# Kernel optimization log

Hardware: AMD Instinct MI355X
Metric: run time of the kernel (lower is better)

The kernel has to match this reference:

```python
import jax, jax.numpy as jnp
import numpy as np

B, L, D = 4, 8192, 512


def _normalize(v):
    # F.normalize: v / max(||v||, 1e-12)
    n = jnp.linalg.norm(v, axis=-1, keepdims=True)
    return v / jnp.maximum(n, 1e-12)


def setup_inputs() -> dict:
    key = jax.random.key(0)
    k1, k2, k3, k4 = jax.random.split(key, 4)
    return {
        "hidden_states": jax.random.normal(k1, (B, L, D), jnp.float32),
        "residual": jax.random.normal(k2, (B, L, D), jnp.float32),
        "q_weight": jax.random.normal(k3, (D, D), jnp.float32) * 0.02,
        "k_weight": jax.random.normal(k4, (D, D), jnp.float32) * 0.02,
        "det_state": jnp.zeros((B, D), jnp.float32),
    }


def reference(hidden_states, residual, q_weight, k_weight, det_state):
    Bs, Ls, Ds = hidden_states.shape
    # ---- CosineSimRouter.prob_boundary ----
    q = _normalize(hidden_states[:, :-1] @ q_weight.T)   # (B, L-1, D)
    k = _normalize(hidden_states[:, 1:] @ k_weight.T)    # (B, L-1, D)
    cos_sim = jnp.einsum('bld,bld->bl', q, k)            # (B, L-1)
    prob = jnp.concatenate(
        [jnp.ones((Bs, 1), jnp.float32), jnp.clip((1.0 - cos_sim) / 2.0, 0.0, 1.0)],
        axis=1)                                           # (B, L); prob[:,0]=1 (state=None path)
    token_mask = prob > 0.5                               # (B, L)

    # ---- Tokenizer: compact boundary positions (pad M -> L, static shape) ----
    counts = token_mask.sum(axis=1)                       # (B,)
    order = jnp.argsort(~token_mask, axis=1)              # stable: True-mask indices first, in order
    valid = jnp.arange(Ls)[None, :] < counts[:, None]     # (B, L)
    chunked = jnp.take_along_axis(hidden_states, order[..., None], axis=1)
    chunked = chunked * valid[..., None]                  # (B, L, D)
    chunk_probs = jnp.take_along_axis(prob, order, axis=1) * valid  # (B, L)

    # ---- DeTokenizer: EMA associative scan over compacted chunks ----
    decay = jnp.clip(1.0 - chunk_probs, 0.0, 1.0)
    # pad positions have chunk_probs=0 -> decay=1 -> state carried unchanged
    a = jnp.broadcast_to(decay[..., None], (Bs, Ls, Ds))
    b = (1.0 - decay)[..., None] * chunked
    b = b.at[:, 0].add(a[:, 0] * det_state)

    def comb(x, y):  # x earlier, y later: (a2*a1, a2*b1 + b2)
        ax, bx = x
        ay, by = y
        return ax * ay, ay * bx + by

    _, ema_out = jax.lax.associative_scan(comb, (a, b), axis=1)
    ema_out = ema_out * valid[..., None]                  # zero padded chunk slots

    # broadcast back to full sequence via cumulative chunk indexing
    chunk_idx = jnp.cumsum(token_mask.astype(jnp.int32), axis=1) - 1  # (B, L)
    ci = jnp.clip(chunk_idx, 0, Ls - 1)
    long_states = jnp.take_along_axis(ema_out, ci[..., None], axis=1)
    long_states = long_states * (chunk_idx >= 0)[..., None]

    # STE coefficient: forward == 1 (grad flows through max(1-p, p) in bwd)
    coef_raw = jnp.maximum(1.0 - prob, prob)
    coef = coef_raw + jax.lax.stop_gradient(1.0 - coef_raw)
    long_states = long_states * coef[..., None]

    output = residual + long_states                       # (B, L, D)
    return output
```

## Files before the change

### kernel.cpp

```cpp
#include <hip/hip_runtime.h>
#include <hip/hip_bf16.h>
#include <math.h>

#define B_  4
#define L_  8192
#define D_  512

#define BM   128
#define NCT  4
#define NRT  (L_ / BM)
#define KW   64
#define NSTAGE (D_ / KW)

#define CHUNK 64
#define NCHUNK (L_ / CHUNK)

#define MAXFIX 16380
#define FIX_TAU 1.0e-3f
#define FTILE 4

typedef short bf16x8 __attribute__((ext_vector_type(8)));
typedef float f32x4 __attribute__((ext_vector_type(4)));
typedef unsigned short u16;
typedef unsigned int u32;

__device__ __forceinline__ u32 pk2(float lo, float hi) {
    __hip_bfloat162 v = __float22bfloat162_rn(float2{lo, hi});
    union { __hip_bfloat162 b; u32 u; } cv; cv.b = v;
    return cv.u;
}

__global__ __launch_bounds__(256) void prep_w(
    const float* __restrict__ wq, const float* __restrict__ wk,
    u16* __restrict__ qh, u16* __restrict__ kh,
    float* __restrict__ wqt, float* __restrict__ wkt,
    int* __restrict__ fix_cnt)
{
    __shared__ float tile[64][65];
    const int bi = blockIdx.x;
    const int bj = blockIdx.y;
    const int t = threadIdx.x;
    if (bi == 0 && bj == 0 && t == 0) *fix_cnt = 0;
    const int c0 = bi * 64, k0 = bj * 64;
    const float* src = wq; float* dst = wqt; u16* dsth = qh;
#pragma unroll
    for (int m = 0; m < 2; ++m) {
        __syncthreads();
#pragma unroll
        for (int it = 0; it < 4; ++it) {
            int r = it * 16 + (t >> 4);
            int cc = (t & 15) * 4;
            float4 v = *(const float4*)(src + (size_t)(c0 + r) * D_ + k0 + cc);
            tile[r][cc] = v.x; tile[r][cc + 1] = v.y;
            tile[r][cc + 2] = v.z; tile[r][cc + 3] = v.w;
            uint2 hv; hv.x = pk2(v.x, v.y); hv.y = pk2(v.z, v.w);
            *(uint2*)(dsth + (size_t)(c0 + r) * D_ + k0 + cc) = hv;
        }
        __syncthreads();
#pragma unroll
        for (int it = 0; it < 4; ++it) {
            int cl = t & 63;
            int kq = it * 4 + (t >> 6);
            float4 v;
            v.x = tile[cl][kq * 4 + 0]; v.y = tile[cl][kq * 4 + 1];
            v.z = tile[cl][kq * 4 + 2]; v.w = tile[cl][kq * 4 + 3];
            size_t o = ((size_t)((k0 >> 2) + kq) * 512 + (c0 + cl)) * 4;
            *(float4*)(dst + o) = v;
        }
        src = wk; dst = wkt; dsth = kh;
    }
}

__global__ __launch_bounds__(256, 2) void qk_mfma(
    const float* __restrict__ h,
    const u16* __restrict__ wqh, const u16* __restrict__ wkh,
    float* __restrict__ part)
{
    const int bid = blockIdx.x;
    const int swz = (bid & 7) * 128 + (bid >> 3);
    const int ct = swz & 3, rt = (swz >> 2) & 63, b = swz >> 8;
    const int t = threadIdx.x, wid = t >> 6, lane = t & 63;
    const int l15 = lane & 15, l4 = lane >> 4;

    __shared__ __align__(16) u16 ah[129 * 64];
    __shared__ float red[4][BM][3];

    const int r0 = rt * BM;
    const float* hb = h + (size_t)b * L_ * D_;

    const int tr = t >> 4, q = t & 15;
    const float* gp = hb + (size_t)(r0 + tr) * D_ + q * 4;
    const int re = (r0 + BM > L_ - 1) ? (L_ - 1) : (r0 + BM);
    const float* gpe = hb + (size_t)re * D_ + q * 4;
    const int dbase = tr * 64 + (((q >> 1) ^ (tr & 7)) * 8) + ((q & 1) * 4);
    const int dE = 128 * 64 + ((t >> 1) * 8) + ((t & 1) * 4);

    const int colb = ct * 128 + wid * 32;
    const u16* bq0 = wqh + (size_t)(colb + l15) * D_ + l4 * 8;
    const u16* bq1 = bq0 + (size_t)16 * D_;
    const u16* bk0 = wkh + (size_t)(colb + l15) * D_ + l4 * 8;
    const u16* bk1 = bk0 + (size_t)16 * D_;

    int aoff[8];
#pragma unroll
    for (int rf = 0; rf < 8; ++rf) {
        int R = rf * 16 + l15;
        aoff[rf] = R * 64 + ((l4 ^ (R & 7)) * 8);
    }
    const int aoffE = 128 * 64 + l4 * 8;

    f32x4 accq[8][2], acck[8][2], ackl[2];
    const f32x4 zero = {0.f, 0.f, 0.f, 0.f};
#pragma unroll
    for (int rf = 0; rf < 8; ++rf) {
        accq[rf][0] = zero; accq[rf][1] = zero;
        acck[rf][0] = zero; acck[rf][1] = zero;
    }
    ackl[0] = zero; ackl[1] = zero;

    float4 A0, A1, A2, A3, A4, A5, A6, A7;
    float4 AE = {0.f, 0.f, 0.f, 0.f};

#define LOADA(S) do { const int _o = (S) * KW;                      \
    A0 = *(const float4*)(gp + _o);                                 \
    A1 = *(const float4*)(gp + _o + 8192);                          \
    A2 = *(const float4*)(gp + _o + 16384);                         \
    A3 = *(const float4*)(gp + _o + 24576);                         \
    A4 = *(const float4*)(gp + _o + 32768);                         \
    A5 = *(const float4*)(gp + _o + 40960);                         \
    A6 = *(const float4*)(gp + _o + 49152);                         \
    A7 = *(const float4*)(gp + _o + 57344);                         \
    if (t < 16) AE = *(const float4*)(gpe + _o); } while (0)

#define ST1(J, AV) { uint2 _h; _h.x = pk2(AV.x, AV.y); _h.y = pk2(AV.z, AV.w); \
    *(uint2*)(&ah[dbase + (J) * 1024]) = _h; }

    LOADA(0);
    for (int s = 0; s < NSTAGE; ++s) {
        __syncthreads();
        ST1(0, A0) ST1(1, A1) ST1(2, A2) ST1(3, A3)
        ST1(4, A4) ST1(5, A5) ST1(6, A6) ST1(7, A7)
        if (t < 16) { uint2 _h; _h.x = pk2(AE.x, AE.y); _h.y = pk2(AE.z, AE.w);
                      *(uint2*)(&ah[dE]) = _h; }

        const int so = s * KW;
        bf16x8 q00 = *(const bf16x8*)(bq0 + so);
        bf16x8 q01 = *(const bf16x8*)(bq0 + so + 32);
        bf16x8 q10 = *(const bf16x8*)(bq1 + so);
        bf16x8 q11 = *(const bf16x8*)(bq1 + so + 32);
        bf16x8 k00 = *(const bf16x8*)(bk0 + so);
        bf16x8 k01 = *(const bf16x8*)(bk0 + so + 32);
        bf16x8 k10 = *(const bf16x8*)(bk1 + so);
        bf16x8 k11 = *(const bf16x8*)(bk1 + so + 32);

        if (s + 1 < NSTAGE) LOADA(s + 1);
        __syncthreads();

#pragma unroll
        for (int kk = 0; kk < 2; ++kk) {
            bf16x8 fq0 = kk ? q01 : q00;
            bf16x8 fq1 = kk ? q11 : q10;
            bf16x8 fk0 = kk ? k01 : k00;
            bf16x8 fk1 = kk ? k11 : k10;
#pragma unroll
            for (int rf = 0; rf < 8; ++rf) {
                bf16x8 a = *(const bf16x8*)(&ah[aoff[rf] ^ (kk * 32)]);
                accq[rf][0] = __builtin_amdgcn_mfma_f32_16x16x32_bf16(a, fq0, accq[rf][0], 0, 0, 0);
                accq[rf][1] = __builtin_amdgcn_mfma_f32_16x16x32_bf16(a, fq1, accq[rf][1], 0, 0, 0);
                acck[rf][0] = __builtin_amdgcn_mfma_f32_16x16x32_bf16(a, fk0, acck[rf][0], 0, 0, 0);
                acck[rf][1] = __builtin_amdgcn_mfma_f32_16x16x32_bf16(a, fk1, acck[rf][1], 0, 0, 0);
            }
            bf16x8 al = *(const bf16x8*)(&ah[aoffE ^ (kk * 32)]);
            ackl[0] = __builtin_amdgcn_mfma_f32_16x16x32_bf16(al, fk0, ackl[0], 0, 0, 0);
            ackl[1] = __builtin_amdgcn_mfma_f32_16x16x32_bf16(al, fk1, ackl[1], 0, 0, 0);
        }
    }
#undef LOADA
#undef ST1

#pragma unroll
    for (int rf = 0; rf < 8; ++rf) {
#pragma unroll
        for (int reg = 0; reg < 4; ++reg) {
            float pq = 0.f, pk = 0.f, pd = 0.f;
#pragma unroll
            for (int cf = 0; cf < 2; ++cf) {
                float qv = accq[rf][cf][reg];
                float kv = acck[rf][cf][reg];
                pq += qv * qv;
                pk += kv * kv;
                float ksh;
                if (reg < 3) {
                    ksh = acck[rf][cf][reg + 1];
                } else {
                    float up = __shfl(acck[rf][cf][0], (lane + 16) & 63);
                    float nx0 = (rf < 7) ? acck[rf + 1][cf][0] : ackl[cf][0];
                    float nx = __shfl(nx0, l15);
                    ksh = (l4 == 3) ? nx : up;
                }
                pd += qv * ksh;
            }
#pragma unroll
            for (int off = 1; off < 16; off <<= 1) {
                pq += __shfl_xor(pq, off);
                pk += __shfl_xor(pk, off);
                pd += __shfl_xor(pd, off);
            }
            if (l15 == 0) {
                int row = rf * 16 + l4 * 4 + reg;
                red[wid][row][0] = pq;
                red[wid][row][1] = pk;
                red[wid][row][2] = pd;
            }
        }
    }
    __syncthreads();
    if (t < BM) {
        float pq = red[0][t][0] + red[1][t][0] + red[2][t][0] + red[3][t][0];
        float pk = red[0][t][1] + red[1][t][1] + red[2][t][1] + red[3][t][1];
        float pd = red[0][t][2] + red[1][t][2] + red[2][t][2] + red[3][t][2];
        size_t o = (((size_t)ct * B_ + b) * L_ + (r0 + t)) * 3;
        part[o + 0] = pq; part[o + 1] = pk; part[o + 2] = pd;
    }
}

__global__ __launch_bounds__(256) void cos_reduce(
    const float* __restrict__ part, float* __restrict__ p,
    int* __restrict__ fix_cnt, int* __restrict__ fix_list)
{
    int idx = blockIdx.x * 256 + threadIdx.x;
    if (idx >= B_ * L_) return;
    int b = idx / L_;
    int tp = idx % L_;
    if (tp == 0) { p[idx] = 1.0f; return; }
    int l = tp - 1;
    float nq = 0.f, nk = 0.f, dt = 0.f;
#pragma unroll
    for (int ct = 0; ct < NCT; ++ct) {
        size_t o = (((size_t)ct * B_ + b) * L_ + l) * 3;
        nq += part[o + 0];
        dt += part[o + 2];
        nk += part[o + 4];
    }
    float qn = sqrtf(nq); if (qn < 1e-12f) qn = 1e-12f;
    float kn = sqrtf(nk); if (kn < 1e-12f) kn = 1e-12f;
    float cs = dt / (qn * kn);
    float pr = 0.5f * (1.0f - cs);
    pr = fminf(fmaxf(pr, 0.0f), 1.0f);
    p[idx] = pr;
    if (fabsf(cs) < FIX_TAU) {
        int slot = atomicAdd(fix_cnt, 1);
        if (slot < MAXFIX) fix_list[slot] = idx;
    }
}

__global__ __launch_bounds__(256) void fixup_main(
    const float* __restrict__ h,
    const float* __restrict__ wqt, const float* __restrict__ wkt,
    const int* __restrict__ fix_cnt, const int* __restrict__ fix_list,
    float* __restrict__ p)
{
    __shared__ float hq[FTILE][D_];
    __shared__ float hk[FTILE][D_];
    __shared__ float red[FTILE][3][4];
    const int t = threadIdx.x, wid = t >> 6, lane = t & 63;
    int n = *fix_cnt; if (n > MAXFIX) n = MAXFIX;
    const int ntiles = (n + FTILE - 1) / FTILE;

    for (int tile = blockIdx.x; tile < ntiles; tile += gridDim.x) {
        __syncthreads();
#pragma unroll
        for (int r = 0; r < FTILE; ++r) {
            int s = tile * FTILE + r;
            int idx = fix_list[s < n ? s : 0];
            int bb = idx >> 13;
            int tp = idx & (L_ - 1);
            const float* hr = h + ((size_t)bb * L_ + (tp - 1)) * D_;
            ((float2*)hq[r])[t] = ((const float2*)hr)[t];
            ((float2*)hk[r])[t] = ((const float2*)(hr + D_))[t];
        }
        __syncthreads();

        float qa0[FTILE], qa1[FTILE], ka0[FTILE], ka1[FTILE];
#pragma unroll
        for (int r = 0; r < FTILE; ++r) { qa0[r] = qa1[r] = ka0[r] = ka1[r] = 0.f; }

        float4 wc0 = *(const float4*)(wqt + ((size_t)0 * 512 + t) * 4);
        float4 wc1 = *(const float4*)(wqt + ((size_t)0 * 512 + t + 256) * 4);
        float4 xc0 = *(const float4*)(wkt + ((size_t)0 * 512 + t) * 4);
        float4 xc1 = *(const float4*)(wkt + ((size_t)0 * 512 + t + 256) * 4);
#pragma unroll 4
        for (int kq = 0; kq < D_ / 4; ++kq) {
            const int kn = (kq + 1) & (D_ / 4 - 1);
            float4 wn0 = *(const float4*)(wqt + ((size_t)kn * 512 + t) * 4);
            float4 wn1 = *(const float4*)(wqt + ((size_t)kn * 512 + t + 256) * 4);
            float4 xn0 = *(const float4*)(wkt + ((size_t)kn * 512 + t) * 4);
            float4 xn1 = *(const float4*)(wkt + ((size_t)kn * 512 + t + 256) * 4);
#pragma unroll
            for (int r = 0; r < FTILE; ++r) {
                float4 hv = *(const float4*)(&hq[r][kq * 4]);
                float4 kv = *(const float4*)(&hk[r][kq * 4]);
                qa0[r] += hv.x * wc0.x + hv.y * wc0.y + hv.z * wc0.z + hv.w * wc0.w;
                qa1[r] += hv.x * wc1.x + hv.y * wc1.y + hv.z * wc1.z + hv.w * wc1.w;
                ka0[r] += kv.x * xc0.x + kv.y * xc0.y + kv.z * xc0.z + kv.w * xc0.w;
                ka1[r] += kv.x * xc1.x + kv.y * xc1.y + kv.z * xc1.z + kv.w * xc1.w;
            }
            wc0 = wn0; wc1 = wn1; xc0 = xn0; xc1 = xn1;
        }

#pragma unroll
        for (int r = 0; r < FTILE; ++r) {
            float pq = qa0[r] * qa0[r] + qa1[r] * qa1[r];
            float pk = ka0[r] * ka0[r] + ka1[r] * ka1[r];
            float pd = qa0[r] * ka0[r] + qa1[r] * ka1[r];
#pragma unroll
            for (int off = 1; off < 64; off <<= 1) {
                pq += __shfl_xor(pq, off);
                pk += __shfl_xor(pk, off);
                pd += __shfl_xor(pd, off);
            }
            if (lane == 0) { red[r][0][wid] = pq; red[r][1][wid] = pk; red[r][2][wid] = pd; }
        }
        __syncthreads();
        if (t < FTILE) {
            int s = tile * FTILE + t;
            if (s < n) {
                float nq = red[t][0][0] + red[t][0][1] + red[t][0][2] + red[t][0][3];
                float nk = red[t][1][0] + red[t][1][1] + red[t][1][2] + red[t][1][3];
                float dt = red[t][2][0] + red[t][2][1] + red[t][2][2] + red[t][2][3];
                float qn = sqrtf(nq); if (qn < 1e-12f) qn = 1e-12f;
                float kn = sqrtf(nk); if (kn < 1e-12f) kn = 1e-12f;
                float cs = dt / (qn * kn);
                float pr = 0.5f * (1.0f - cs);
                pr = fminf(fmaxf(pr, 0.0f), 1.0f);
                p[fix_list[s]] = pr;
            }
        }
    }
}

__global__ __launch_bounds__(256) void scan_a(
    const float* __restrict__ h, const float* __restrict__ p,
    float* __restrict__ Bc, float* __restrict__ Ac)
{
    const int t = threadIdx.x;
    const int c = blockIdx.x, b = blockIdx.y;
    const int l0 = c * CHUNK;
    const float* pb = p + (size_t)b * L_ + l0;
    const float2* hb = (const float2*)(h + ((size_t)b * L_ + l0) * D_) + t;

    float2 st = {0.f, 0.f};
    float ap = 1.f;
#pragma unroll 4
    for (int i = 0; i < CHUNK; ++i) {
        float pr = pb[i];
        float2 hv = hb[(size_t)i * 256];
        bool sel = pr > 0.5f;
        float a = sel ? 1.f - pr : 1.f;
        float g = sel ? pr : 0.f;
        st.x = a * st.x + g * hv.x;
        st.y = a * st.y + g * hv.y;
        ap *= a;
    }
    ((float2*)Bc)[((size_t)b * NCHUNK + c) * 256 + t] = st;
    if (t == 0) Ac[b * NCHUNK + c] = ap;
}

__global__ __launch_bounds__(256) void scan_b(
    const float* __restrict__ Ac, const float* __restrict__ Bc,
    const float* __restrict__ det, float* __restrict__ carry)
{
    const int t = threadIdx.x;
    const int b = blockIdx.x;
    const float* acb = Ac + b * NCHUNK;
    const float2* bcb = (const float2*)Bc + (size_t)b * NCHUNK * 256 + t;
    float2* cb = (float2*)carry + (size_t)b * NCHUNK * 256 + t;
    float2 st = ((const float2*)det)[(size_t)b * 256 + t];

    float a0 = acb[0], a1 = acb[1], a2 = acb[2], a3 = acb[3];
    float2 b0 = bcb[0], b1 = bcb[256], b2 = bcb[512], b3 = bcb[768];
    for (int g = 0; g < NCHUNK / 4; ++g) {
        const int nc = (g + 1 < NCHUNK / 4) ? (g + 1) * 4 : g * 4;
        float an0 = acb[nc], an1 = acb[nc + 1], an2 = acb[nc + 2], an3 = acb[nc + 3];
        float2 bn0 = bcb[(size_t)nc * 256],        bn1 = bcb[(size_t)(nc + 1) * 256];
        float2 bn2 = bcb[(size_t)(nc + 2) * 256],  bn3 = bcb[(size_t)(nc + 3) * 256];
        const size_t c0 = (size_t)g * 4 * 256;
        cb[c0]       = st; st.x = a0 * st.x + b0.x; st.y = a0 * st.y + b0.y;
        cb[c0 + 256] = st; st.x = a1 * st.x + b1.x; st.y = a1 * st.y + b1.y;
        cb[c0 + 512] = st; st.x = a2 * st.x + b2.x; st.y = a2 * st.y + b2.y;
        cb[c0 + 768] = st; st.x = a3 * st.x + b3.x; st.y = a3 * st.y + b3.y;
        a0 = an0; a1 = an1; a2 = an2; a3 = an3;
        b0 = bn0; b1 = bn1; b2 = bn2; b3 = bn3;
    }
}

__global__ __launch_bounds__(256) void scan_c(
    const float* __restrict__ h, const float* __restrict__ p,
    const float* __restrict__ res, const float* __restrict__ carry,
    float* __restrict__ out)
{
    const int t = threadIdx.x;
    const int c = blockIdx.x, b = blockIdx.y;
    const int l0 = c * CHUNK;
    const float* pb = p + (size_t)b * L_ + l0;
    const size_t base = ((size_t)b * L_ + l0) * 256 + t;
    const float2* hb = (const float2*)h + base;
    const float2* rb = (const float2*)res + base;
    float2* ob = (float2*)out + base;

    float2 st = ((const float2*)carry)[((size_t)b * NCHUNK + c) * 256 + t];
#pragma unroll 4
    for (int i = 0; i < CHUNK; ++i) {
        float pr = pb[i];
        float2 hv = hb[(size_t)i * 256];
        float2 rv = rb[(size_t)i * 256];
        bool sel = pr > 0.5f;
        float a = sel ? 1.f - pr : 1.f;
        float g = sel ? pr : 0.f;
        st.x = a * st.x + g * hv.x;
        st.y = a * st.y + g * hv.y;
        float2 ov; ov.x = rv.x + st.x; ov.y = rv.y + st.y;
        ob[(size_t)i * 256] = ov;
    }
}

extern "C" void kernel_launch(void* const* d_in, const int* in_sizes, int n_in,
                              void* d_out, int out_size, void* d_ws, size_t ws_size,
                              hipStream_t stream)
{
    const float* h   = (const float*)d_in[0];
    const float* res = (const float*)d_in[1];
    const float* wq  = (const float*)d_in[2];
    const float* wk  = (const float*)d_in[3];
    const float* det = (const float*)d_in[4];
    float* out = (float*)d_out;

    float* ws = (float*)d_ws;
    float* part  = ws;
    float* p     = part + (size_t)NCT * B_ * L_ * 3;
    float* Ac    = p + (size_t)B_ * L_;
    float* Bc    = Ac + (size_t)B_ * NCHUNK;
    float* carry = Bc + (size_t)B_ * NCHUNK * D_;
    int*  fix_cnt  = (int*)(carry + (size_t)B_ * NCHUNK * D_);
    int*  fix_list = fix_cnt + 4;
    u16* wqh = (u16*)(fix_list + MAXFIX);
    u16* wkh = wqh + (size_t)D_ * D_;
    float* wqt = (float*)(wkh + (size_t)D_ * D_);
    float* wkt = wqt + (size_t)D_ * D_;

    prep_w<<<dim3(8, 8), 256, 0, stream>>>(wq, wk, wqh, wkh, wqt, wkt, fix_cnt);
    qk_mfma<<<NCT * NRT * B_, 256, 0, stream>>>(h, wqh, wkh, part);
    cos_reduce<<<(B_ * L_ + 255) / 256, 256, 0, stream>>>(part, p, fix_cnt, fix_list);
    fixup_main<<<256, 256, 0, stream>>>(h, wqt, wkt, fix_cnt, fix_list, p);
    scan_a<<<dim3(NCHUNK, B_), 256, 0, stream>>>(h, p, Bc, Ac);
    scan_b<<<B_, 256, 0, stream>>>(Ac, Bc, det, carry);
    scan_c<<<dim3(NCHUNK, B_), 256, 0, stream>>>(h, p, res, carry, out);
}
```

Measured before the change: 201.7 us.

## Tune fixup tiling, software-pipeline weight loads, relax barriers, prefetch weights into cache

Several changes at once. The fixup kernel now processes 8 rows per tile on half as many blocks and uses a 4-deep rotating register pipeline for weight loads. The MFMA kernel swaps __syncthreads for raw s_barrier with an explicit lgkmcnt wait and sched barriers. cos_reduce reads the transposed fp32 weights purely to warm L2 before fixup runs. The aim is to hide load latency and amortise weight traffic, at the cost of more registers and extra loads in cos_reduce.

```diff
diff --git a/kernel.cpp b/kernel.cpp
--- a/kernel.cpp
+++ b/kernel.cpp
@@ -17,7 +17,7 @@
 
 #define MAXFIX 16380
 #define FIX_TAU 1.0e-3f
-#define FTILE 4
+#define FTILE 8
 
 typedef short bf16x8 __attribute__((ext_vector_type(8)));
 typedef float f32x4 __attribute__((ext_vector_type(4)));
@@ -137,7 +137,10 @@
 
     LOADA(0);
     for (int s = 0; s < NSTAGE; ++s) {
-        __syncthreads();
+        __builtin_amdgcn_sched_barrier(0);
+        __builtin_amdgcn_s_barrier();
+        __builtin_amdgcn_sched_barrier(0);
+
         ST1(0, A0) ST1(1, A1) ST1(2, A2) ST1(3, A3)
         ST1(4, A4) ST1(5, A5) ST1(6, A6) ST1(7, A7)
         if (t < 16) { uint2 _h; _h.x = pk2(AE.x, AE.y); _h.y = pk2(AE.z, AE.w);
@@ -154,7 +157,11 @@
         bf16x8 k11 = *(const bf16x8*)(bk1 + so + 32);
 
         if (s + 1 < NSTAGE) LOADA(s + 1);
-        __syncthreads();
+
+        asm volatile("s_waitcnt lgkmcnt(0)" ::: "memory");
+        __builtin_amdgcn_sched_barrier(0);
+        __builtin_amdgcn_s_barrier();
+        __builtin_amdgcn_sched_barrier(0);
 
 #pragma unroll
         for (int kk = 0; kk < 2; ++kk) {
@@ -226,10 +233,17 @@
 
 __global__ __launch_bounds__(256) void cos_reduce(
     const float* __restrict__ part, float* __restrict__ p,
-    int* __restrict__ fix_cnt, int* __restrict__ fix_list)
+    int* __restrict__ fix_cnt, int* __restrict__ fix_list,
+    const float* __restrict__ wqt, const float* __restrict__ wkt)
 {
     int idx = blockIdx.x * 256 + threadIdx.x;
     if (idx >= B_ * L_) return;
+    {
+        const float4* a = (const float4*)wqt + (size_t)idx * 2;
+        const float4* c = (const float4*)wkt + (size_t)idx * 2;
+        float4 v0 = a[0], v1 = a[1], u0 = c[0], u1 = c[1];
+        asm volatile("" :: "v"(v0.x), "v"(v1.x), "v"(u0.x), "v"(u1.x));
+    }
     int b = idx / L_;
     int tp = idx % L_;
     if (tp == 0) { p[idx] = 1.0f; return; }
@@ -285,28 +299,39 @@
 #pragma unroll
         for (int r = 0; r < FTILE; ++r) { qa0[r] = qa1[r] = ka0[r] = ka1[r] = 0.f; }
 
-        float4 wc0 = *(const float4*)(wqt + ((size_t)0 * 512 + t) * 4);
-        float4 wc1 = *(const float4*)(wqt + ((size_t)0 * 512 + t + 256) * 4);
-        float4 xc0 = *(const float4*)(wkt + ((size_t)0 * 512 + t) * 4);
-        float4 xc1 = *(const float4*)(wkt + ((size_t)0 * 512 + t + 256) * 4);
-#pragma unroll 4
-        for (int kq = 0; kq < D_ / 4; ++kq) {
-            const int kn = (kq + 1) & (D_ / 4 - 1);
-            float4 wn0 = *(const float4*)(wqt + ((size_t)kn * 512 + t) * 4);
-            float4 wn1 = *(const float4*)(wqt + ((size_t)kn * 512 + t + 256) * 4);
-            float4 xn0 = *(const float4*)(wkt + ((size_t)kn * 512 + t) * 4);
-            float4 xn1 = *(const float4*)(wkt + ((size_t)kn * 512 + t + 256) * 4);
-#pragma unroll
-            for (int r = 0; r < FTILE; ++r) {
-                float4 hv = *(const float4*)(&hq[r][kq * 4]);
-                float4 kv = *(const float4*)(&hk[r][kq * 4]);
-                qa0[r] += hv.x * wc0.x + hv.y * wc0.y + hv.z * wc0.z + hv.w * wc0.w;
-                qa1[r] += hv.x * wc1.x + hv.y * wc1.y + hv.z * wc1.z + hv.w * wc1.w;
-                ka0[r] += kv.x * xc0.x + kv.y * xc0.y + kv.z * xc0.z + kv.w * xc0.w;
-                ka1[r] += kv.x * xc1.x + kv.y * xc1.y + kv.z * xc1.z + kv.w * xc1.w;
-            }
-            wc0 = wn0; wc1 = wn1; xc0 = xn0; xc1 = xn1;
-        }
+#define LDW(SET, KQ) do { const int _k = (KQ);                              \
+    w0##SET = *(const float4*)(wqt + ((size_t)_k * 512 + t) * 4);           \
+    w1##SET = *(const float4*)(wqt + ((size_t)_k * 512 + t + 256) * 4);     \
+    x0##SET = *(const float4*)(wkt + ((size_t)_k * 512 + t) * 4);           \
+    x1##SET = *(const float4*)(wkt + ((size_t)_k * 512 + t + 256) * 4); } while (0)
+
+#define FMA_STEP(KQ, W0, W1, X0, X1) do {                                   \
+    _Pragma("unroll")                                                       \
+    for (int r = 0; r < FTILE; ++r) {                                       \
+        float4 hv = *(const float4*)(&hq[r][(KQ) * 4]);                     \
+        float4 kv = *(const float4*)(&hk[r][(KQ) * 4]);                     \
+        qa0[r] += hv.x * W0.x + hv.y * W0.y + hv.z * W0.z + hv.w * W0.w;    \
+        qa1[r] += hv.x * W1.x + hv.y * W1.y + hv.z * W1.z + hv.w * W1.w;    \
+        ka0[r] += kv.x * X0.x + kv.y * X0.y + kv.z * X0.z + kv.w * X0.w;    \
+        ka1[r] += kv.x * X1.x + kv.y * X1.y + kv.z * X1.z + kv.w * X1.w;    \
+    } } while (0)
+
+        float4 w0A, w1A, x0A, x1A, w0B, w1B, x0B, x1B;
+        float4 w0C, w1C, x0C, x1C, w0D, w1D, x0D, x1D;
+        LDW(A, 0); LDW(B, 1); LDW(C, 2); LDW(D, 3);
+        for (int g = 0; g < 32; ++g) {
+            const int base = g * 4;
+            FMA_STEP(base + 0, w0A, w1A, x0A, x1A);
+            { int nk_ = base + 4; if (nk_ > 127) nk_ = 127; LDW(A, nk_); }
+            FMA_STEP(base + 1, w0B, w1B, x0B, x1B);
+            { int nk_ = base + 5; if (nk_ > 127) nk_ = 127; LDW(B, nk_); }
+            FMA_STEP(base + 2, w0C, w1C, x0C, x1C);
+            { int nk_ = base + 6; if (nk_ > 127) nk_ = 127; LDW(C, nk_); }
+            FMA_STEP(base + 3, w0D, w1D, x0D, x1D);
+            { int nk_ = base + 7; if (nk_ > 127) nk_ = 127; LDW(D, nk_); }
+        }
+#undef LDW
+#undef FMA_STEP
 
 #pragma unroll
         for (int r = 0; r < FTILE; ++r) {
@@ -450,8 +475,8 @@
 
     prep_w<<<dim3(8, 8), 256, 0, stream>>>(wq, wk, wqh, wkh, wqt, wkt, fix_cnt);
     qk_mfma<<<NCT * NRT * B_, 256, 0, stream>>>(h, wqh, wkh, part);
-    cos_reduce<<<(B_ * L_ + 255) / 256, 256, 0, stream>>>(part, p, fix_cnt, fix_list);
-    fixup_main<<<256, 256, 0, stream>>>(h, wqt, wkt, fix_cnt, fix_list, p);
+    cos_reduce<<<(B_ * L_ + 255) / 256, 256, 0, stream>>>(part, p, fix_cnt, fix_list, wqt, wkt);
+    fixup_main<<<128, 256, 0, stream>>>(h, wqt, wkt, fix_cnt, fix_list, p);
     scan_a<<<dim3(NCHUNK, B_), 256, 0, stream>>>(h, p, Bc, Ac);
     scan_b<<<B_, 256, 0, stream>>>(Ac, Bc, det, carry);
     scan_c<<<dim3(NCHUNK, B_), 256, 0, stream>>>(h, p, res, carry, out);
```

Result: slower. 243.7 us (+20.8%).
